# Kernel optimization log

Hardware: AMD Instinct MI355X
Metric: run time of the kernel (lower is better)

## Reference

```python
import jax, jax.numpy as jnp
import numpy as np

EPS = 1e-06
TEMP = 2.0

def _l2norm(x, eps=EPS):
    # F.normalize: x / max(||x||, eps)
    n = jnp.sqrt(jnp.sum(x * x, axis=-1, keepdims=True))
    return x / jnp.maximum(n, eps)

def setup_inputs() -> dict:
    key = jax.random.key(0)
    k1, k2 = jax.random.split(key)
    B, Lt, Lv, D = 8, 64, 16384, 256
    t = jax.random.normal(k1, (B, Lt, D), dtype=jnp.float32)
    v = jax.random.normal(k2, (B, Lv, D), dtype=jnp.float32)
    return {"t": t, "v": v}

def reference(t, v):
    dtype = v.dtype
    t = _l2norm(jnp.nan_to_num(t).astype(jnp.float32))
    v = _l2norm(jnp.nan_to_num(v).astype(jnp.float32))
    # S: [B, Lv, Lt]
    S = jnp.einsum('bvd,btd->bvt', v, t) / TEMP
    # text->vision attention: softmax over text axis (stable shift as in source)
    S_vt = jnp.nan_to_num(S - jnp.max(S, axis=2, keepdims=True))
    A_vt = jax.nn.softmax(S_vt, axis=2)            # [B, Lv, Lt]
    weights_vt = jax.nn.softmax(A_vt / TEMP, axis=1)  # softmax over vision axis
    text_score = jnp.sum(weights_vt * A_vt, axis=1)   # [B, Lt]
    text_score = text_score / (jnp.sum(text_score, axis=1, keepdims=True) + EPS)
    # vision<-text attention: per-sample loop in source == batched softmax over Lv
    S_tv = jnp.nan_to_num(S - jnp.max(S, axis=1, keepdims=True))
    A_tv = jax.nn.softmax(S_tv, axis=1)            # softmax over vision axis, [B, Lv, Lt]
    scores = jnp.einsum('bvt,bt->bv', A_tv, text_score)  # [B, Lv]
    mn = jnp.min(scores, axis=1, keepdims=True)
    mx = jnp.max(scores, axis=1, keepdims=True)
    scores = (scores - mn) / (mx - mn + EPS)
    return scores.astype(dtype)
```

## Files before the change

### kernel.cpp

```cpp
#include <hip/hip_runtime.h>
#include <stdint.h>

#define NB 8
#define LT 64
#define LV 16384
#define DD 256
#define EPSV 1e-6f
#define BF16MAX 3.3895313892515355e38f

typedef unsigned short u16t;
typedef __attribute__((ext_vector_type(8))) short short8;
typedef __attribute__((ext_vector_type(4))) float floatx4;

__device__ __forceinline__ float bf2f(u16t h) {
    union { uint32_t u; float f; } cv; cv.u = ((uint32_t)h) << 16; return cv.f;
}
__device__ __forceinline__ uint32_t asu(float f) { union { float f; uint32_t u; } c; c.f = f; return c.u; }
__device__ __forceinline__ float asf(uint32_t u) { union { uint32_t u; float f; } c; c.u = u; return c.f; }
__device__ __forceinline__ u16t f2bf(float f) {
    uint32_t u = asu(f);
    return (u16t)((u + 0x7fffu + ((u >> 16) & 1u)) >> 16);
}
__device__ __forceinline__ float fixnum(float f) {
    if (f != f) return 0.0f;
    if (f > BF16MAX) return BF16MAX;
    if (f < -BF16MAX) return -BF16MAX;
    return f;
}
__device__ __forceinline__ float load_in(const void* p, long i, int isf32) {
    return isf32 ? ((const float*)p)[i] : bf2f(((const u16t*)p)[i]);
}
__device__ __forceinline__ uint32_t bfhead(float a, float& hf) {
    uint32_t u = asu(a);
    uint32_t h = (u + 0x7fffu + ((u >> 16) & 1u)) >> 16;
    hf = asf(h << 16);
    return h;
}

__global__ void k_sniff(const u16t* v, int* flag) {
    int lane = threadIdx.x;
    int sane = 0;
    for (int i = 0; i < 16; ++i) {
        u16t h = v[lane * 16 + i];
        int ex = (h >> 7) & 0xFF;
        if ((h & 0x7FFF) == 0 || (ex >= 96 && ex < 160)) ++sane;
    }
    #pragma unroll
    for (int o = 1; o < 64; o <<= 1) sane += __shfl_xor(sane, o, 64);
    if (lane == 0) flag[0] = (sane < 900) ? 1 : 0;
}

__global__ void k0_zero(float* Z) {
    int i = blockIdx.x * 256 + threadIdx.x;
    if (i < 1536) Z[i] = 0.0f;
}

__global__ void k1_tnorm(const void* t, u16t* tnB, const int* flag) {
    __shared__ float red[256];
    int isf32 = flag[0];
    int row = blockIdx.x;
    int k = threadIdx.x;
    float x = fixnum(load_in(t, (long)row * DD + k, isf32));
    red[k] = x * x;
    __syncthreads();
    for (int s = 128; s > 0; s >>= 1) {
        if (k < s) red[k] += red[k + s];
        __syncthreads();
    }
    float scale = 0.5f / fmaxf(sqrtf(red[0]), EPSV);
    tnB[row * DD + k] = f2bf(x * scale);
}

__global__ __launch_bounds__(256) void k_gemm(const void* v, const u16t* tnB,
                                              float* Z, float* S1, float* S2,
                                              const float* c, float* scores,
                                              const int* flag, int mode) {
    __shared__ u16t ldsT[64 * 264];
    __shared__ float zlds[3][4][64];
    int isf32 = flag[0];
    int tid = threadIdx.x, wave = tid >> 6, lane = tid & 63;
    int c16 = lane & 15, q = lane >> 4;
    int b = blockIdx.y, tile = blockIdx.x;
    int rowbase = tile * 128 + wave * 32;

    {
        const u16t* src = tnB + (size_t)b * (LT * DD);
        for (int i = tid; i < 2048; i += 256) {
            int tt = i >> 5, k8 = i & 31;
            *(uint4*)&ldsT[tt * 264 + k8 * 8] = *(const uint4*)&src[tt * DD + k8 * 8];
        }
    }
    __syncthreads();

    floatx4 acc[2][4];
    #pragma unroll
    for (int mt = 0; mt < 2; ++mt)
        #pragma unroll
        for (int nt = 0; nt < 4; ++nt) acc[mt][nt] = (floatx4){0.f, 0.f, 0.f, 0.f};
    float ssqp[2] = {0.f, 0.f};

    for (int kc = 0; kc < 8; ++kc) {
        short8 bf[4];
        #pragma unroll
        for (int nt = 0; nt < 4; ++nt)
            bf[nt] = *(const short8*)&ldsT[(nt * 16 + c16) * 264 + kc * 32 + q * 8];

        #pragma unroll
        for (int mt = 0; mt < 2; ++mt) {
            int row = rowbase + mt * 16 + c16;
            float f[8];
            if (isf32) {
                const float* vr = (const float*)v +
                    ((size_t)b * LV + row) * DD + kc * 32 + q * 8;
                float4 p0 = *(const float4*)vr;
                float4 p1 = *(const float4*)(vr + 4);
                f[0]=p0.x; f[1]=p0.y; f[2]=p0.z; f[3]=p0.w;
                f[4]=p1.x; f[5]=p1.y; f[6]=p1.z; f[7]=p1.w;
            } else {
                const u16t* vr = (const u16t*)v +
                    ((size_t)b * LV + row) * DD + kc * 32 + q * 8;
                uint4 u = *(const uint4*)vr;
                f[0]=bf2f((u16t)u.x); f[1]=bf2f((u16t)(u.x>>16));
                f[2]=bf2f((u16t)u.y); f[3]=bf2f((u16t)(u.y>>16));
                f[4]=bf2f((u16t)u.z); f[5]=bf2f((u16t)(u.z>>16));
                f[6]=bf2f((u16t)u.w); f[7]=bf2f((u16t)(u.w>>16));
            }
            #pragma unroll
            for (int i = 0; i < 8; ++i) f[i] = fixnum(f[i]);
            union { short8 s; uint32_t u[4]; } a1, a2, a3;
            #pragma unroll
            for (int i = 0; i < 4; ++i) {
                float e0 = f[2*i], e1 = f[2*i+1];
                ssqp[mt] += e0 * e0 + e1 * e1;
                float h10f, h11f, h20f, h21f, dummy;
                uint32_t h10 = bfhead(e0, h10f), h11 = bfhead(e1, h11f);
                float r10 = e0 - h10f,  r11 = e1 - h11f;
                uint32_t h20 = bfhead(r10, h20f), h21 = bfhead(r11, h21f);
                float r20 = r10 - h20f, r21 = r11 - h21f;
                uint32_t h30 = bfhead(r20, dummy), h31 = bfhead(r21, dummy);
                a1.u[i] = h10 | (h11 << 16);
                a2.u[i] = h20 | (h21 << 16);
                a3.u[i] = h30 | (h31 << 16);
            }
            #pragma unroll
            for (int nt = 0; nt < 4; ++nt) {
                acc[mt][nt] = __builtin_amdgcn_mfma_f32_16x16x32_bf16(
                    a1.s, bf[nt], acc[mt][nt], 0, 0, 0);
                acc[mt][nt] = __builtin_amdgcn_mfma_f32_16x16x32_bf16(
                    a2.s, bf[nt], acc[mt][nt], 0, 0, 0);
                acc[mt][nt] = __builtin_amdgcn_mfma_f32_16x16x32_bf16(
                    a3.s, bf[nt], acc[mt][nt], 0, 0, 0);
            }
        }
    }

    float ssqf[2];
    #pragma unroll
    for (int mt = 0; mt < 2; ++mt) {
        float s = ssqp[mt];
        s += __shfl_xor(s, 16, 64);
        s += __shfl_xor(s, 32, 64);
        ssqf[mt] = s;
    }
    float facr[2][4];
    #pragma unroll
    for (int mt = 0; mt < 2; ++mt)
        #pragma unroll
        for (int reg = 0; reg < 4; ++reg) {
            float ss = __shfl(ssqf[mt], q * 4 + reg, 64);
            facr[mt][reg] = 1.0f / fmaxf(sqrtf(ss), EPSV);
        }

    if (mode == 0) {
        float zacc[4] = {0,0,0,0}, s1acc[4] = {0,0,0,0}, s2acc[4] = {0,0,0,0};
        #pragma unroll
        for (int mt = 0; mt < 2; ++mt)
            #pragma unroll
            for (int reg = 0; reg < 4; ++reg) {
                float e[4], se = 0.f;
                #pragma unroll
                for (int nt = 0; nt < 4; ++nt) {
                    e[nt] = __expf(acc[mt][nt][reg] * facr[mt][reg]);
                    se += e[nt];
                }
                se += __shfl_xor(se, 1, 64);
                se += __shfl_xor(se, 2, 64);
                se += __shfl_xor(se, 4, 64);
                se += __shfl_xor(se, 8, 64);
                float inv = 1.0f / se;
                #pragma unroll
                for (int nt = 0; nt < 4; ++nt) {
                    float A = e[nt] * inv;
                    float w = __expf(0.5f * A);
                    zacc[nt] += e[nt]; s1acc[nt] += w; s2acc[nt] += w * A;
                }
            }
        #pragma unroll
        for (int nt = 0; nt < 4; ++nt) {
            zacc[nt]  += __shfl_xor(zacc[nt], 16, 64);  zacc[nt]  += __shfl_xor(zacc[nt], 32, 64);
            s1acc[nt] += __shfl_xor(s1acc[nt], 16, 64); s1acc[nt] += __shfl_xor(s1acc[nt], 32, 64);
            s2acc[nt] += __shfl_xor(s2acc[nt], 16, 64); s2acc[nt] += __shfl_xor(s2acc[nt], 32, 64);
        }
        if (lane < 16) {
            #pragma unroll
            for (int nt = 0; nt < 4; ++nt) {
                zlds[0][wave][nt * 16 + lane] = zacc[nt];
                zlds[1][wave][nt * 16 + lane] = s1acc[nt];
                zlds[2][wave][nt * 16 + lane] = s2acc[nt];
            }
        }
        __syncthreads();
        if (tid < 64) {
            float z  = zlds[0][0][tid] + zlds[0][1][tid] + zlds[0][2][tid] + zlds[0][3][tid];
            float a  = zlds[1][0][tid] + zlds[1][1][tid] + zlds[1][2][tid] + zlds[1][3][tid];
            float s2 = zlds[2][0][tid] + zlds[2][1][tid] + zlds[2][2][tid] + zlds[2][3][tid];
            atomicAdd(&Z[b * LT + tid], z);
            atomicAdd(&S1[b * LT + tid], a);
            atomicAdd(&S2[b * LT + tid], s2);
        }
    } else {
        float cc[4];
        #pragma unroll
        for (int nt = 0; nt < 4; ++nt) cc[nt] = c[b * LT + nt * 16 + c16];
        #pragma unroll
        for (int mt = 0; mt < 2; ++mt)
            #pragma unroll
            for (int reg = 0; reg < 4; ++reg) {
                float x = 0.f;
                #pragma unroll
                for (int nt = 0; nt < 4; ++nt)
                    x += __expf(acc[mt][nt][reg] * facr[mt][reg]) * cc[nt];
                x += __shfl_xor(x, 1, 64);
                x += __shfl_xor(x, 2, 64);
                x += __shfl_xor(x, 4, 64);
                x += __shfl_xor(x, 8, 64);
                if (c16 == 0)
                    scores[(size_t)b * LV + rowbase + mt * 16 + q * 4 + reg] = x;
            }
    }
}

__global__ __launch_bounds__(64) void k3_coef(const float* Z, const float* S1,
                                              const float* S2, float* c) {
    int b = blockIdx.x, lane = threadIdx.x;
    float ts = S2[b * LT + lane] / S1[b * LT + lane];
    float tot = ts;
    #pragma unroll
    for (int o = 1; o < 64; o <<= 1) tot += __shfl_xor(tot, o, 64);
    c[b * LT + lane] = ts / ((tot + EPSV) * Z[b * LT + lane]);
}

__global__ __launch_bounds__(256) void k_mnmx(const float* scores, float* mnmx) {
    __shared__ float rmn[256], rmx[256];
    int b = blockIdx.x, tid = threadIdx.x;
    float mn = 3.4e38f, mx = -3.4e38f;
    for (int i = tid; i < LV; i += 256) {
        float x = scores[b * LV + i];
        mn = fminf(mn, x); mx = fmaxf(mx, x);
    }
    rmn[tid] = mn; rmx[tid] = mx;
    __syncthreads();
    for (int s = 128; s > 0; s >>= 1) {
        if (tid < s) {
            rmn[tid] = fminf(rmn[tid], rmn[tid + s]);
            rmx[tid] = fmaxf(rmx[tid], rmx[tid + s]);
        }
        __syncthreads();
    }
    if (tid == 0) { mnmx[b * 2] = rmn[0]; mnmx[b * 2 + 1] = rmx[0]; }
}

__global__ __launch_bounds__(256) void k5_out(const float* scores, const float* mnmx,
                                              void* out, const int* flag) {
    int isf32 = flag[0];
    int i = blockIdx.x * 256 + threadIdx.x;
    if (i >= NB * LV) return;
    int b = i >> 14;
    float mn = mnmx[b * 2], mx = mnmx[b * 2 + 1];
    float val = (scores[i] - mn) / (mx - mn + EPSV);
    if (isf32) ((float*)out)[i] = val;
    else ((u16t*)out)[i] = f2bf(val);
}

extern "C" void kernel_launch(void* const* d_in, const int* in_sizes, int n_in,
                              void* d_out, int out_size, void* d_ws, size_t ws_size,
                              hipStream_t stream) {
    const void* t = d_in[0];
    const void* v = d_in[1];
    char* w = (char*)d_ws;

    u16t*  tnB    = (u16t*)w;
    float* scores = (float*)(w + 262144);
    float* Z      = (float*)(w + 786432);
    float* S1     = Z + 512;
    float* S2     = Z + 1024;
    float* c      = Z + 1536;
    float* mnmx   = Z + 2048;
    int*   flag   = (int*)(Z + 2064);

    k_sniff<<<1, 64, 0, stream>>>((const u16t*)v, flag);
    k0_zero<<<6, 256, 0, stream>>>(Z);
    k1_tnorm<<<512, 256, 0, stream>>>(t, tnB, flag);
    k_gemm<<<dim3(128, NB), 256, 0, stream>>>(v, tnB, Z, S1, S2, nullptr, nullptr, flag, 0);
    k3_coef<<<NB, 64, 0, stream>>>(Z, S1, S2, c);
    k_gemm<<<dim3(128, NB), 256, 0, stream>>>(v, tnB, Z, S1, S2, c, scores, flag, 1);
    k_mnmx<<<NB, 256, 0, stream>>>(scores, mnmx);
    k5_out<<<512, 256, 0, stream>>>(scores, mnmx, d_out, flag);
}
```

Baseline: 266.2 us.

## Materialize exp scores once instead of recomputing GEMM in second pass

The second GEMM pass over v is replaced by storing the per-row exponentials from the first pass into a workspace buffer. A new lightweight kernel reads that buffer, applies the text coefficients and computes per-batch min/max with atomics. The separate min/max kernel is removed and the init kernels are merged. This removes a full re-read of v and the repeated matmul, at the cost of writing and reading a 32 MB intermediate.

```diff
diff --git a/kernel.cpp b/kernel.cpp
--- a/kernel.cpp
+++ b/kernel.cpp
@@ -37,22 +37,22 @@
     return h;
 }
 
-__global__ void k_sniff(const u16t* v, int* flag) {
-    int lane = threadIdx.x;
-    int sane = 0;
-    for (int i = 0; i < 16; ++i) {
-        u16t h = v[lane * 16 + i];
-        int ex = (h >> 7) & 0xFF;
-        if ((h & 0x7FFF) == 0 || (ex >= 96 && ex < 160)) ++sane;
-    }
-    #pragma unroll
-    for (int o = 1; o < 64; o <<= 1) sane += __shfl_xor(sane, o, 64);
-    if (lane == 0) flag[0] = (sane < 900) ? 1 : 0;
-}
-
-__global__ void k0_zero(float* Z) {
-    int i = blockIdx.x * 256 + threadIdx.x;
-    if (i < 1536) Z[i] = 0.0f;
+__global__ __launch_bounds__(256) void k_init(const u16t* v, float* Z,
+                                              uint32_t* mnmx, int* flag) {
+    int tid = threadIdx.x;
+    for (int i = tid; i < 1536; i += 256) Z[i] = 0.0f;
+    if (tid < NB) { mnmx[tid * 2] = 0x7f800000u; mnmx[tid * 2 + 1] = 0u; }
+    if (tid < 64) {
+        int sane = 0;
+        for (int i = 0; i < 16; ++i) {
+            u16t h = v[tid * 16 + i];
+            int ex = (h >> 7) & 0xFF;
+            if ((h & 0x7FFF) == 0 || (ex >= 96 && ex < 160)) ++sane;
+        }
+        #pragma unroll
+        for (int o = 1; o < 64; o <<= 1) sane += __shfl_xor(sane, o, 64);
+        if (tid == 0) flag[0] = (sane < 900) ? 1 : 0;
+    }
 }
 
 __global__ void k1_tnorm(const void* t, u16t* tnB, const int* flag) {
@@ -72,9 +72,8 @@
 }
 
 __global__ __launch_bounds__(256) void k_gemm(const void* v, const u16t* tnB,
-                                              float* Z, float* S1, float* S2,
-                                              const float* c, float* scores,
-                                              const int* flag, int mode) {
+                                              float* Sc, float* Z, float* S1,
+                                              float* S2, const int* flag) {
     __shared__ u16t ldsT[64 * 264];
     __shared__ float zlds[3][4][64];
     int isf32 = flag[0];
@@ -171,72 +170,53 @@
             facr[mt][reg] = 1.0f / fmaxf(sqrtf(ss), EPSV);
         }
 
-    if (mode == 0) {
-        float zacc[4] = {0,0,0,0}, s1acc[4] = {0,0,0,0}, s2acc[4] = {0,0,0,0};
-        #pragma unroll
-        for (int mt = 0; mt < 2; ++mt)
-            #pragma unroll
-            for (int reg = 0; reg < 4; ++reg) {
-                float e[4], se = 0.f;
-                #pragma unroll
-                for (int nt = 0; nt < 4; ++nt) {
-                    e[nt] = __expf(acc[mt][nt][reg] * facr[mt][reg]);
-                    se += e[nt];
-                }
-                se += __shfl_xor(se, 1, 64);
-                se += __shfl_xor(se, 2, 64);
-                se += __shfl_xor(se, 4, 64);
-                se += __shfl_xor(se, 8, 64);
-                float inv = 1.0f / se;
-                #pragma unroll
-                for (int nt = 0; nt < 4; ++nt) {
-                    float A = e[nt] * inv;
-                    float w = __expf(0.5f * A);
-                    zacc[nt] += e[nt]; s1acc[nt] += w; s2acc[nt] += w * A;
-                }
-            }
+    float zacc[4] = {0,0,0,0}, s1acc[4] = {0,0,0,0}, s2acc[4] = {0,0,0,0};
+    #pragma unroll
+    for (int mt = 0; mt < 2; ++mt)
+        #pragma unroll
+        for (int reg = 0; reg < 4; ++reg) {
+            float e[4], se = 0.f;
+            #pragma unroll
+            for (int nt = 0; nt < 4; ++nt) {
+                e[nt] = __expf(acc[mt][nt][reg] * facr[mt][reg]);
+                se += e[nt];
+            }
+            se += __shfl_xor(se, 1, 64);
+            se += __shfl_xor(se, 2, 64);
+            se += __shfl_xor(se, 4, 64);
+            se += __shfl_xor(se, 8, 64);
+            float inv = 1.0f / se;
+            size_t srow = (size_t)b * LV + rowbase + mt * 16 + q * 4 + reg;
+            #pragma unroll
+            for (int nt = 0; nt < 4; ++nt) {
+                Sc[srow * LT + nt * 16 + c16] = e[nt];
+                float A = e[nt] * inv;
+                float w = __expf(0.5f * A);
+                zacc[nt] += e[nt]; s1acc[nt] += w; s2acc[nt] += w * A;
+            }
+        }
+    #pragma unroll
+    for (int nt = 0; nt < 4; ++nt) {
+        zacc[nt]  += __shfl_xor(zacc[nt], 16, 64);  zacc[nt]  += __shfl_xor(zacc[nt], 32, 64);
+        s1acc[nt] += __shfl_xor(s1acc[nt], 16, 64); s1acc[nt] += __shfl_xor(s1acc[nt], 32, 64);
+        s2acc[nt] += __shfl_xor(s2acc[nt], 16, 64); s2acc[nt] += __shfl_xor(s2acc[nt], 32, 64);
+    }
+    if (lane < 16) {
         #pragma unroll
         for (int nt = 0; nt < 4; ++nt) {
-            zacc[nt]  += __shfl_xor(zacc[nt], 16, 64);  zacc[nt]  += __shfl_xor(zacc[nt], 32, 64);
-            s1acc[nt] += __shfl_xor(s1acc[nt], 16, 64); s1acc[nt] += __shfl_xor(s1acc[nt], 32, 64);
-            s2acc[nt] += __shfl_xor(s2acc[nt], 16, 64); s2acc[nt] += __shfl_xor(s2acc[nt], 32, 64);
-        }
-        if (lane < 16) {
-            #pragma unroll
-            for (int nt = 0; nt < 4; ++nt) {
-                zlds[0][wave][nt * 16 + lane] = zacc[nt];
-                zlds[1][wave][nt * 16 + lane] = s1acc[nt];
-                zlds[2][wave][nt * 16 + lane] = s2acc[nt];
-            }
-        }
-        __syncthreads();
-        if (tid < 64) {
-            float z  = zlds[0][0][tid] + zlds[0][1][tid] + zlds[0][2][tid] + zlds[0][3][tid];
-            float a  = zlds[1][0][tid] + zlds[1][1][tid] + zlds[1][2][tid] + zlds[1][3][tid];
-            float s2 = zlds[2][0][tid] + zlds[2][1][tid] + zlds[2][2][tid] + zlds[2][3][tid];
-            atomicAdd(&Z[b * LT + tid], z);
-            atomicAdd(&S1[b * LT + tid], a);
-            atomicAdd(&S2[b * LT + tid], s2);
-        }
-    } else {
-        float cc[4];
-        #pragma unroll
-        for (int nt = 0; nt < 4; ++nt) cc[nt] = c[b * LT + nt * 16 + c16];
-        #pragma unroll
-        for (int mt = 0; mt < 2; ++mt)
-            #pragma unroll
-            for (int reg = 0; reg < 4; ++reg) {
-                float x = 0.f;
-                #pragma unroll
-                for (int nt = 0; nt < 4; ++nt)
-                    x += __expf(acc[mt][nt][reg] * facr[mt][reg]) * cc[nt];
-                x += __shfl_xor(x, 1, 64);
-                x += __shfl_xor(x, 2, 64);
-                x += __shfl_xor(x, 4, 64);
-                x += __shfl_xor(x, 8, 64);
-                if (c16 == 0)
-                    scores[(size_t)b * LV + rowbase + mt * 16 + q * 4 + reg] = x;
-            }
+            zlds[0][wave][nt * 16 + lane] = zacc[nt];
+            zlds[1][wave][nt * 16 + lane] = s1acc[nt];
+            zlds[2][wave][nt * 16 + lane] = s2acc[nt];
+        }
+    }
+    __syncthreads();
+    if (tid < 64) {
+        float z  = zlds[0][0][tid] + zlds[0][1][tid] + zlds[0][2][tid] + zlds[0][3][tid];
+        float a  = zlds[1][0][tid] + zlds[1][1][tid] + zlds[1][2][tid] + zlds[1][3][tid];
+        float s2 = zlds[2][0][tid] + zlds[2][1][tid] + zlds[2][2][tid] + zlds[2][3][tid];
+        atomicAdd(&Z[b * LT + tid], z);
+        atomicAdd(&S1[b * LT + tid], a);
+        atomicAdd(&S2[b * LT + tid], s2);
     }
 }
 
@@ -250,33 +230,40 @@
     c[b * LT + lane] = ts / ((tot + EPSV) * Z[b * LT + lane]);
 }
 
-__global__ __launch_bounds__(256) void k_mnmx(const float* scores, float* mnmx) {
-    __shared__ float rmn[256], rmx[256];
-    int b = blockIdx.x, tid = threadIdx.x;
-    float mn = 3.4e38f, mx = -3.4e38f;
-    for (int i = tid; i < LV; i += 256) {
-        float x = scores[b * LV + i];
+__global__ __launch_bounds__(256) void k4_scores(const float* Sc, const float* c,
+                                                 float* scores, uint32_t* mnmx) {
+    __shared__ float bmn[4], bmx[4];
+    int tid = threadIdx.x, wave = tid >> 6, lane = tid & 63;
+    int rowbase = blockIdx.x * 32 + wave * 8;
+    int b = rowbase >> 14;
+    float cr = c[b * LT + lane];
+    float mn = 3.4e38f, mx = 0.f;
+    #pragma unroll
+    for (int g = 0; g < 8; ++g) {
+        int row = rowbase + g;
+        float x = Sc[(size_t)row * LT + lane] * cr;
+        #pragma unroll
+        for (int o = 1; o < 64; o <<= 1) x += __shfl_xor(x, o, 64);
+        if (lane == 0) scores[row] = x;
         mn = fminf(mn, x); mx = fmaxf(mx, x);
     }
-    rmn[tid] = mn; rmx[tid] = mx;
-    __syncthreads();
-    for (int s = 128; s > 0; s >>= 1) {
-        if (tid < s) {
-            rmn[tid] = fminf(rmn[tid], rmn[tid + s]);
-            rmx[tid] = fmaxf(rmx[tid], rmx[tid + s]);
-        }
-        __syncthreads();
-    }
-    if (tid == 0) { mnmx[b * 2] = rmn[0]; mnmx[b * 2 + 1] = rmx[0]; }
-}
-
-__global__ __launch_bounds__(256) void k5_out(const float* scores, const float* mnmx,
+    if (lane == 0) { bmn[wave] = mn; bmx[wave] = mx; }
+    __syncthreads();
+    if (tid == 0) {
+        float m0 = fminf(fminf(bmn[0], bmn[1]), fminf(bmn[2], bmn[3]));
+        float m1 = fmaxf(fmaxf(bmx[0], bmx[1]), fmaxf(bmx[2], bmx[3]));
+        atomicMin(&mnmx[b * 2], asu(m0));
+        atomicMax(&mnmx[b * 2 + 1], asu(m1));
+    }
+}
+
+__global__ __launch_bounds__(256) void k5_out(const float* scores, const uint32_t* mnmx,
                                               void* out, const int* flag) {
     int isf32 = flag[0];
     int i = blockIdx.x * 256 + threadIdx.x;
     if (i >= NB * LV) return;
     int b = i >> 14;
-    float mn = mnmx[b * 2], mx = mnmx[b * 2 + 1];
+    float mn = asf(mnmx[b * 2]), mx = asf(mnmx[b * 2 + 1]);
     float val = (scores[i] - mn) / (mx - mn + EPSV);
     if (isf32) ((float*)out)[i] = val;
     else ((u16t*)out)[i] = f2bf(val);
@@ -289,21 +276,20 @@
     const void* v = d_in[1];
     char* w = (char*)d_ws;
 
-    u16t*  tnB    = (u16t*)w;
-    float* scores = (float*)(w + 262144);
-    float* Z      = (float*)(w + 786432);
-    float* S1     = Z + 512;
-    float* S2     = Z + 1024;
-    float* c      = Z + 1536;
-    float* mnmx   = Z + 2048;
-    int*   flag   = (int*)(Z + 2064);
-
-    k_sniff<<<1, 64, 0, stream>>>((const u16t*)v, flag);
-    k0_zero<<<6, 256, 0, stream>>>(Z);
+    float*    Sc     = (float*)w;
+    u16t*     tnB    = (u16t*)(w + 33554432);
+    float*    scores = (float*)(w + 33816576);
+    float*    Z      = (float*)(w + 34340864);
+    float*    S1     = Z + 512;
+    float*    S2     = Z + 1024;
+    float*    c      = Z + 1536;
+    uint32_t* mnmx   = (uint32_t*)(Z + 2048);
+    int*      flag   = (int*)(Z + 2064);
+
+    k_init<<<1, 256, 0, stream>>>((const u16t*)v, Z, mnmx, flag);
     k1_tnorm<<<512, 256, 0, stream>>>(t, tnB, flag);
-    k_gemm<<<dim3(128, NB), 256, 0, stream>>>(v, tnB, Z, S1, S2, nullptr, nullptr, flag, 0);
+    k_gemm<<<dim3(128, NB), 256, 0, stream>>>(v, tnB, Sc, Z, S1, S2, flag);
     k3_coef<<<NB, 64, 0, stream>>>(Z, S1, S2, c);
-    k_gemm<<<dim3(128, NB), 256, 0, stream>>>(v, tnB, Z, S1, S2, c, scores, flag, 1);
-    k_mnmx<<<NB, 256, 0, stream>>>(scores, mnmx);
+    k4_scores<<<4096, 256, 0, stream>>>(Sc, c, scores, mnmx);
     k5_out<<<512, 256, 0, stream>>>(scores, mnmx, d_out, flag);
 }
```

Result: slower. 316.9 us (+19.0%).
